# Optimization experiments

Hardware: AMD Instinct MI355X
Metric: run time of the kernel (lower is better)

The kernel has to match this reference:

```python
import jax, jax.numpy as jnp
import numpy as np

N_NODES = 50000
N_EDGES = 400000
D = 300          # num_features == hidden_units
L = 5            # num_layers
C = 128          # num_outputs
NG = 256         # graphs per batch
BN_EPS = 1e-5


def setup_inputs() -> dict:
    key = jax.random.key(0)
    ks = jax.random.split(key, 16)
    x = jax.random.normal(ks[0], (N_NODES, D), dtype=jnp.float32)
    edge_index = jax.random.randint(ks[1], (2, N_EDGES), 0, N_NODES, dtype=jnp.int64)
    batch = jnp.sort(jax.random.randint(ks[2], (N_NODES,), 0, NG, dtype=jnp.int64))
    s = 1.0 / np.sqrt(D)
    # Stacked per-layer GINConv MLP params: Linear -> BN -> ReLU -> Linear, then outer BN
    mlp_W1 = jax.random.uniform(ks[3], (L, D, D), jnp.float32, -s, s)
    mlp_b1 = jax.random.uniform(ks[4], (L, D), jnp.float32, -s, s)
    mlp_g1 = jnp.ones((L, D), jnp.float32)
    mlp_be1 = jnp.zeros((L, D), jnp.float32)
    mlp_W2 = jax.random.uniform(ks[5], (L, D, D), jnp.float32, -s, s)
    mlp_b2 = jax.random.uniform(ks[6], (L, D), jnp.float32, -s, s)
    bn_g = jnp.ones((L, D), jnp.float32)
    bn_b = jnp.zeros((L, D), jnp.float32)
    # num_layers+1 readout heads (num_features == hidden_units so all [D, C])
    fc_W = jax.random.uniform(ks[7], (L + 1, D, C), jnp.float32, -s, s)
    fc_b = jax.random.uniform(ks[8], (L + 1, C), jnp.float32, -s, s)
    return dict(x=x, edge_index=edge_index, batch=batch,
                mlp_W1=mlp_W1, mlp_b1=mlp_b1, mlp_g1=mlp_g1, mlp_be1=mlp_be1,
                mlp_W2=mlp_W2, mlp_b2=mlp_b2, bn_g=bn_g, bn_b=bn_b,
                fc_W=fc_W, fc_b=fc_b)


def _bn(h, gamma, beta):
    # BatchNorm1d in training mode: biased batch stats over the node dim
    mu = h.mean(axis=0)
    var = h.var(axis=0)
    return (h - mu) * jax.lax.rsqrt(var + BN_EPS) * gamma + beta


def reference(x, edge_index, batch, mlp_W1, mlp_b1, mlp_g1, mlp_be1,
              mlp_W2, mlp_b2, bn_g, bn_b, fc_W, fc_b):
    src, dst = edge_index[0], edge_index[1]
    n = x.shape[0]
    outs = [x]
    h = x
    for i in range(L):
        # GINConv (eps=0): MLP(x + sum_{j in N(i)} x_j), scatter-add over edges
        agg = jax.ops.segment_sum(h[src], dst, num_segments=n)
        z = h + agg
        z = z @ mlp_W1[i] + mlp_b1[i]
        z = jax.nn.relu(_bn(z, mlp_g1[i], mlp_be1[i]))
        z = z @ mlp_W2[i] + mlp_b2[i]
        h = jax.nn.relu(_bn(z, bn_g[i], bn_b[i]))  # outer BN + ReLU
        outs.append(h)
    # global mean pool per graph, then per-depth linear heads summed (dropout off in eval)
    counts = jax.ops.segment_sum(jnp.ones((n,), x.dtype), batch, num_segments=NG)
    inv = 1.0 / jnp.maximum(counts, 1.0)
    out = jnp.zeros((NG, C), x.dtype)
    for i, hi in enumerate(outs):
        pooled = jax.ops.segment_sum(hi, batch, num_segments=NG) * inv[:, None]
        out = out + (pooled @ fc_W[i] + fc_b[i])
    return out
```

## Files before the change

kernel.cpp:

```cpp
#include <hip/hip_runtime.h>

#define D 300
#define KP 320
#define NPAD 50048
#define NTILES 782
#define TPB 4
#define GB 196
#define WSTRIDE 328
#define NGR 256
#define NL 5
#define NC 128
#define BN_EPS 1e-5f

typedef __attribute__((ext_vector_type(8))) short bf16x8;
typedef __attribute__((ext_vector_type(4))) float f32x4;
typedef unsigned short u16;

__device__ __forceinline__ void atomAdd(float* p, float v) { unsafeAtomicAdd(p, v); }

__device__ __forceinline__ short f2bf(float f) {
    union { float f; unsigned u; } v; v.f = f;
    unsigned r = v.u + 0x7fffu + ((v.u >> 16) & 1u);
    return (short)(r >> 16);
}
__device__ __forceinline__ float bf2f(short s) {
    union { unsigned u; float f; } v;
    v.u = ((unsigned)(u16)s) << 16;
    return v.f;
}

__global__ void offsets_kernel(const int* __restrict__ batch, int* __restrict__ off, int N) {
    int g = threadIdx.x;
    if (g > NGR) return;
    int lo = 0, hi = N;
    while (lo < hi) {
        int mid = (lo + hi) >> 1;
        if (batch[mid] < g) lo = mid + 1; else hi = mid;
    }
    off[g] = lo;
}

__global__ __launch_bounds__(256)
void deg_kernel(const int* __restrict__ ei, int* __restrict__ deg, int E) {
    int e = blockIdx.x * 256 + threadIdx.x;
    if (e < E) atomicAdd(&deg[ei[E + e]], 1);
}

__global__ __launch_bounds__(256)
void degpart_kernel(const int* __restrict__ deg, int* __restrict__ part, int N) {
    int i = blockIdx.x * 256 + threadIdx.x;
    int v = (i < N) ? deg[i] : 0;
    #pragma unroll
    for (int o = 1; o < 64; o <<= 1) v += __shfl_xor(v, o);
    __shared__ int ws[4];
    if ((threadIdx.x & 63) == 0) ws[threadIdx.x >> 6] = v;
    __syncthreads();
    if (threadIdx.x == 0) part[blockIdx.x] = ws[0] + ws[1] + ws[2] + ws[3];
}

__global__ __launch_bounds__(256)
void partscan_kernel(int* __restrict__ part, int nb) {
    __shared__ int buf[256];
    int t = threadIdx.x;
    int v = (t < nb) ? part[t] : 0;
    buf[t] = v;
    __syncthreads();
    for (int o = 1; o < 256; o <<= 1) {
        int u = (t >= o) ? buf[t - o] : 0;
        __syncthreads();
        buf[t] += u;
        __syncthreads();
    }
    if (t < nb) part[t] = (t == 0) ? 0 : buf[t - 1];
}

__global__ __launch_bounds__(256)
void rowptr_kernel(const int* __restrict__ deg, const int* __restrict__ part,
                   int* __restrict__ rowptr, int N, int E) {
    __shared__ int buf[256];
    int b = blockIdx.x, t = threadIdx.x;
    int i = b * 256 + t;
    int v = (i < N) ? deg[i] : 0;
    buf[t] = v;
    __syncthreads();
    for (int o = 1; o < 256; o <<= 1) {
        int u = (t >= o) ? buf[t - o] : 0;
        __syncthreads();
        buf[t] += u;
        __syncthreads();
    }
    if (i < N) rowptr[i] = part[b] + buf[t] - v;
    if (b == 0 && t == 0) rowptr[N] = E;
}

__global__ __launch_bounds__(256)
void fill_kernel(const int* __restrict__ ei, const int* __restrict__ rowptr,
                 int* __restrict__ cursor, int* __restrict__ col, int E) {
    int e = blockIdx.x * 256 + threadIdx.x;
    if (e >= E) return;
    int src = ei[e];
    int dst = ei[E + e];
    int pos = atomicAdd(&cursor[dst], 1);
    col[rowptr[dst] + pos] = src;
}

__global__ __launch_bounds__(256)
void wcvt_kernel(const float* __restrict__ W1, const float* __restrict__ W2,
                 u16* __restrict__ Wt) {
    int idx = blockIdx.x * 256 + threadIdx.x;
    if (idx >= 10 * KP * 80) return;
    int n4 = idx % 80;
    int k = (idx / 80) % KP;
    int mat = idx / (80 * KP);
    const float* Wsrc = (mat < NL) ? (W1 + (size_t)mat * D * D) : (W2 + (size_t)(mat - NL) * D * D);
    float4 w = make_float4(0.f, 0.f, 0.f, 0.f);
    if (k < D && n4 < 75) w = *(const float4*)(Wsrc + (size_t)k * D + n4 * 4);
    size_t base = ((size_t)mat * 320 + n4 * 4) * KP + k;
    Wt[base]          = (u16)f2bf(w.x);
    Wt[base + KP]     = (u16)f2bf(w.y);
    Wt[base + 2 * KP] = (u16)f2bf(w.z);
    Wt[base + 3 * KP] = (u16)f2bf(w.w);
}

__global__ __launch_bounds__(256)
void xcvt_kernel(const float* __restrict__ x, u16* __restrict__ xbf, int N) {
    int idx = blockIdx.x * 256 + threadIdx.x;
    if (idx >= NPAD * 40) return;
    int row = idx / 40;
    int c8 = (idx - row * 40) * 8;
    short o[8];
    #pragma unroll
    for (int i = 0; i < 8; ++i) {
        int c = c8 + i;
        float f = (row < N && c < D) ? x[(size_t)row * D + c] : 0.f;
        o[i] = f2bf(f);
    }
    *(bf16x8*)(xbf + (size_t)row * KP + c8) = *(bf16x8*)o;
}

template<bool APPLY>
__global__ __launch_bounds__(256)
void gather_kernel(const u16* __restrict__ H, u16* __restrict__ Z,
                   const int* __restrict__ rowptr, const int* __restrict__ col,
                   const float* __restrict__ scsh, int N) {
    int idx = blockIdx.x * 256 + threadIdx.x;
    if (idx >= N * 40) return;
    int node = idx / 40;
    int c8 = (idx - node * 40) * 8;
    float sc[8], sh[8];
    if (APPLY) {
        #pragma unroll
        for (int i = 0; i < 8; ++i) { sc[i] = scsh[c8 + i]; sh[i] = scsh[KP + c8 + i]; }
    }
    int s = rowptr[node], e = rowptr[node + 1];
    bf16x8 v = *(const bf16x8*)(H + (size_t)node * KP + c8);
    float acc[8];
    #pragma unroll
    for (int i = 0; i < 8; ++i) {
        float f = bf2f(v[i]);
        acc[i] = APPLY ? fmaxf(fmaf(f, sc[i], sh[i]), 0.f) : f;
    }
    int j = s;
    for (; j + 2 <= e; j += 2) {
        int s0 = col[j], s1 = col[j + 1];
        bf16x8 w0 = *(const bf16x8*)(H + (size_t)s0 * KP + c8);
        bf16x8 w1 = *(const bf16x8*)(H + (size_t)s1 * KP + c8);
        #pragma unroll
        for (int i = 0; i < 8; ++i) {
            float f0 = bf2f(w0[i]);
            float f1 = bf2f(w1[i]);
            acc[i] += APPLY ? fmaxf(fmaf(f0, sc[i], sh[i]), 0.f) : f0;
            acc[i] += APPLY ? fmaxf(fmaf(f1, sc[i], sh[i]), 0.f) : f1;
        }
    }
    if (j < e) {
        int s0 = col[j];
        bf16x8 w0 = *(const bf16x8*)(H + (size_t)s0 * KP + c8);
        #pragma unroll
        for (int i = 0; i < 8; ++i) {
            float f0 = bf2f(w0[i]);
            acc[i] += APPLY ? fmaxf(fmaf(f0, sc[i], sh[i]), 0.f) : f0;
        }
    }
    short o[8];
    #pragma unroll
    for (int i = 0; i < 8; ++i) o[i] = f2bf(acc[i]);
    *(bf16x8*)(Z + (size_t)node * KP + c8) = *(bf16x8*)o;
}

template<bool APPLY>
__global__ __launch_bounds__(320)
void pool_kernel(const u16* __restrict__ H, const int* __restrict__ off,
                 const float* __restrict__ scsh, float* __restrict__ pooled_l) {
    __shared__ float red[8][KP];
    int t = threadIdx.x;
    int g = blockIdx.x;
    int rq = t / 40;
    int c8 = (t - rq * 40) * 8;
    float sc[8], sh[8];
    if (APPLY) {
        #pragma unroll
        for (int i = 0; i < 8; ++i) { sc[i] = scsh[c8 + i]; sh[i] = scsh[KP + c8 + i]; }
    }
    int r0 = off[g], r1 = off[g + 1];
    float a[8] = {};
    for (int r = r0 + rq; r < r1; r += 8) {
        bf16x8 v = *(const bf16x8*)(H + (size_t)r * KP + c8);
        #pragma unroll
        for (int i = 0; i < 8; ++i) {
            float f = bf2f(v[i]);
            a[i] += APPLY ? fmaxf(fmaf(f, sc[i], sh[i]), 0.f) : f;
        }
    }
    #pragma unroll
    for (int i = 0; i < 8; ++i) red[rq][c8 + i] = a[i];
    __syncthreads();
    int c = t;
    if (c < D) {
        float s = 0.f;
        #pragma unroll
        for (int j = 0; j < 8; ++j) s += red[j][c];
        pooled_l[g * D + c] = s;
    }
}

template<bool APPLY>
__global__ __launch_bounds__(256)
void mfma_gemm_kernel(const u16* __restrict__ Abf, const u16* __restrict__ Wt,
                      const float* __restrict__ bias, const float* __restrict__ scsh,
                      u16* __restrict__ Cbf, float* __restrict__ stats, int Nreal) {
    __shared__ u16 Ws[80 * WSTRIDE];
    __shared__ float lsum[80], lsq[80];
    const int tid = threadIdx.x;
    const int nBase = blockIdx.y * 80;

    {
        const u16* src = Wt + (size_t)nBase * KP;
        for (int unit = tid; unit < 80 * 40; unit += 256) {
            int n = unit / 40, kg = unit - n * 40;
            *(bf16x8*)&Ws[n * WSTRIDE + kg * 8] =
                *(const bf16x8*)(src + (size_t)n * KP + kg * 8);
        }
    }
    if (tid < 80) { lsum[tid] = 0.f; lsq[tid] = 0.f; }
    __syncthreads();

    const int wave = tid >> 6, lane = tid & 63;
    const int quad = lane >> 4, l16 = lane & 15;

    for (int t = 0; t < TPB; ++t) {
        const int tile = blockIdx.x * TPB + t;
        if (tile >= NTILES) break;
        const int mBase = tile * 64 + wave * 16;
        const u16* arow = Abf + (size_t)(mBase + l16) * KP + quad * 8;

        bf16x8 a[10];
        #pragma unroll
        for (int kc = 0; kc < 10; ++kc) a[kc] = *(const bf16x8*)(arow + kc * 32);
        if (APPLY) {
            #pragma unroll
            for (int kc = 0; kc < 10; ++kc) {
                const float* sp = scsh + kc * 32 + quad * 8;
                float4 s0 = *(const float4*)sp;
                float4 s1 = *(const float4*)(sp + 4);
                float4 h0 = *(const float4*)(sp + KP);
                float4 h1 = *(const float4*)(sp + KP + 4);
                float sc[8] = {s0.x, s0.y, s0.z, s0.w, s1.x, s1.y, s1.z, s1.w};
                float sh[8] = {h0.x, h0.y, h0.z, h0.w, h1.x, h1.y, h1.z, h1.w};
                short o[8];
                #pragma unroll
                for (int i = 0; i < 8; ++i)
                    o[i] = f2bf(fmaxf(fmaf(bf2f(a[kc][i]), sc[i], sh[i]), 0.f));
                a[kc] = *(bf16x8*)o;
            }
        }

        f32x4 acc[5] = {};
        #pragma unroll
        for (int kc = 0; kc < 10; ++kc) {
            #pragma unroll
            for (int nt = 0; nt < 5; ++nt) {
                bf16x8 b = *(const bf16x8*)&Ws[(nt * 16 + l16) * WSTRIDE + kc * 32 + quad * 8];
                acc[nt] = __builtin_amdgcn_mfma_f32_16x16x32_bf16(a[kc], b, acc[nt], 0, 0, 0);
            }
        }

        const int rbase = mBase + quad * 4;
        #pragma unroll
        for (int nt = 0; nt < 5; ++nt) {
            int nl = nt * 16 + l16;
            int colg = nBase + nl;
            if (colg >= D) continue;
            float bia = bias[colg];
            float s = 0.f, q = 0.f;
            #pragma unroll
            for (int r = 0; r < 4; ++r) {
                int row = rbase + r;
                float v = acc[nt][r] + bia;
                bool ok = row < Nreal;
                if (ok) { s += v; q = fmaf(v, v, q); }
                Cbf[(size_t)row * KP + colg] = ok ? (u16)f2bf(v) : (u16)0;
            }
            s += __shfl_xor(s, 16); s += __shfl_xor(s, 32);
            q += __shfl_xor(q, 16); q += __shfl_xor(q, 32);
            if (quad == 0) { atomicAdd(&lsum[nl], s); atomicAdd(&lsq[nl], q); }
        }
    }
    __syncthreads();
    if (tid < 80) {
        int colg = nBase + tid;
        if (colg < D) {
            atomAdd(&stats[colg], lsum[tid]);
            atomAdd(&stats[KP + colg], lsq[tid]);
        }
    }
}

__global__ void bnfin_kernel(float* __restrict__ sums, const float* __restrict__ g,
                             const float* __restrict__ be, float* __restrict__ scsh, float invN) {
    int c = threadIdx.x;
    if (c >= D) return;
    float mu = sums[c] * invN;
    float var = sums[KP + c] * invN - mu * mu;
    float s = g[c] / sqrtf(var + BN_EPS);
    scsh[c] = s;
    scsh[KP + c] = fmaf(-mu, s, be[c]);
    sums[c] = 0.f;
    sums[KP + c] = 0.f;
}

__global__ __launch_bounds__(128)
void bias_init_kernel(const float* __restrict__ fcb, float* __restrict__ out) {
    int i = blockIdx.x * 128 + threadIdx.x;
    if (i >= NGR * NC) return;
    int c = i & (NC - 1);
    float s = 0.f;
    for (int l = 0; l <= NL; ++l) s += fcb[l * NC + c];
    out[i] = s;
}

__global__ __launch_bounds__(128)
void readout_kernel(const float* __restrict__ pooled, const int* __restrict__ off,
                    const float* __restrict__ fcW, float* __restrict__ out) {
    __shared__ float sp[4][D];
    int c = threadIdx.x;
    int l = blockIdx.y;
    int g0 = blockIdx.x * 4;
    for (int i = c; i < 4 * D; i += 128) {
        int gg = i / D, k = i - gg * D;
        sp[gg][k] = pooled[((size_t)l * NGR + g0 + gg) * D + k];
    }
    __syncthreads();
    float acc[4] = {0.f, 0.f, 0.f, 0.f};
    for (int k = 0; k < D; ++k) {
        float w = fcW[((size_t)l * D + k) * NC + c];
        #pragma unroll
        for (int gg = 0; gg < 4; ++gg) acc[gg] = fmaf(sp[gg][k], w, acc[gg]);
    }
    #pragma unroll
    for (int gg = 0; gg < 4; ++gg) {
        int g = g0 + gg;
        float inv = 1.0f / fmaxf((float)(off[g + 1] - off[g]), 1.0f);
        atomAdd(&out[g * NC + c], acc[gg] * inv);
    }
}

extern "C" void kernel_launch(void* const* d_in, const int* in_sizes, int n_in,
                              void* d_out, int out_size, void* d_ws, size_t ws_size,
                              hipStream_t stream) {
    const float* x       = (const float*)d_in[0];
    const int*   ei      = (const int*)d_in[1];
    const int*   batch   = (const int*)d_in[2];
    const float* W1  = (const float*)d_in[3];
    const float* b1  = (const float*)d_in[4];
    const float* g1  = (const float*)d_in[5];
    const float* be1 = (const float*)d_in[6];
    const float* W2  = (const float*)d_in[7];
    const float* b2  = (const float*)d_in[8];
    const float* bng = (const float*)d_in[9];
    const float* bnb = (const float*)d_in[10];
    const float* fcW = (const float*)d_in[11];
    const float* fcb = (const float*)d_in[12];
    float* out = (float*)d_out;

    const int N = in_sizes[0] / D;
    const int E = in_sizes[1] / 2;
    const int nb = (N + 255) / 256;

    u16* xbf  = (u16*)d_ws;
    u16* bufA = xbf + (size_t)NPAD * KP;
    u16* bufB = bufA + (size_t)NPAD * KP;
    u16* Wt   = bufB + (size_t)NPAD * KP;
    float* pooled = (float*)(Wt + (size_t)10 * 320 * KP);
    float* stats  = pooled + (size_t)(NL + 1) * NGR * D;
    float* sc1    = stats + 2 * KP;
    float* sc2    = sc1 + 2 * KP;
    int*   off    = (int*)(sc2 + 2 * KP);
    int*   rowptr = off + NGR + 1;
    int*   cursor = rowptr + N + 1;
    int*   col    = cursor + N;
    int*   part   = col + E;

    hipMemsetAsync(stats, 0, 6 * KP * sizeof(float), stream);
    offsets_kernel<<<1, 320, 0, stream>>>(batch, off, N);
    bias_init_kernel<<<(NGR * NC + 127) / 128, 128, 0, stream>>>(fcb, out);

    hipMemsetAsync(cursor, 0, N * sizeof(int), stream);
    deg_kernel<<<(E + 255) / 256, 256, 0, stream>>>(ei, cursor, E);
    degpart_kernel<<<nb, 256, 0, stream>>>(cursor, part, N);
    partscan_kernel<<<1, 256, 0, stream>>>(part, nb);
    rowptr_kernel<<<nb, 256, 0, stream>>>(cursor, part, rowptr, N, E);
    hipMemsetAsync(cursor, 0, N * sizeof(int), stream);
    fill_kernel<<<(E + 255) / 256, 256, 0, stream>>>(ei, rowptr, cursor, col, E);

    wcvt_kernel<<<(10 * KP * 80 + 255) / 256, 256, 0, stream>>>(W1, W2, Wt);
    xcvt_kernel<<<(NPAD * 40 + 255) / 256, 256, 0, stream>>>(x, xbf, N);

    const dim3 gemm_grid(GB, 4);
    const int nd40 = N * 40;
    float invN = 1.0f / (float)N;
    const size_t WtM = (size_t)320 * KP;

    pool_kernel<false><<<NGR, 320, 0, stream>>>(xbf, off, sc2, pooled);

    u16* g = bufA;
    u16* t = bufB;
    const u16* src = xbf;
    for (int l = 0; l < NL; ++l) {
        if (l == 0)
            gather_kernel<false><<<(nd40 + 255) / 256, 256, 0, stream>>>(src, g, rowptr, col, sc2, N);
        else
            gather_kernel<true><<<(nd40 + 255) / 256, 256, 0, stream>>>(src, g, rowptr, col, sc2, N);
        mfma_gemm_kernel<false><<<gemm_grid, 256, 0, stream>>>(
            g, Wt + (size_t)l * WtM, b1 + l * D, sc1, t, stats, N);
        bnfin_kernel<<<1, 320, 0, stream>>>(stats, g1 + l * D, be1 + l * D, sc1, invN);
        mfma_gemm_kernel<true><<<gemm_grid, 256, 0, stream>>>(
            t, Wt + (size_t)(NL + l) * WtM, b2 + l * D, sc1, g, stats, N);
        bnfin_kernel<<<1, 320, 0, stream>>>(stats, bng + l * D, bnb + l * D, sc2, invN);
        pool_kernel<true><<<NGR, 320, 0, stream>>>(g, off, sc2, pooled + (size_t)(l + 1) * NGR * D);
        src = g;
        u16* tmp = g; g = t; t = tmp;
    }
    readout_kernel<<<dim3(NGR / 4, NL + 1), 128, 0, stream>>>(pooled, off, fcW, out);
}
```

Baseline: 1.094 ms.

## Process 128-row tiles per wave pair with prefetched A fragments in MFMA GEMM

The GEMM kernel now computes two 64-row groups per wave, so each B fragment loaded from LDS feeds two MFMAs. The A fragments for the next tile are loaded during the current tile's MFMA loop, and the first tile's A loads are issued before the weight staging into LDS. Scalar bf16 rounding is replaced with the v_cvt_pk_bf16_f32 packed instruction, and the launch bound requests 3 blocks per SM. The cost is higher register pressure from the doubled A and accumulator arrays, which may reduce occupancy.

```diff
diff --git a/kernel.cpp b/kernel.cpp
--- a/kernel.cpp
+++ b/kernel.cpp
@@ -3,8 +3,8 @@
 #define D 300
 #define KP 320
 #define NPAD 50048
-#define NTILES 782
-#define TPB 4
+#define NT128 391
+#define TPB 2
 #define GB 196
 #define WSTRIDE 328
 #define NGR 256
@@ -27,6 +27,11 @@
     union { unsigned u; float f; } v;
     v.u = ((unsigned)(u16)s) << 16;
     return v.f;
+}
+__device__ __forceinline__ unsigned cvtpk(float lo, float hi) {
+    unsigned r;
+    asm("v_cvt_pk_bf16_f32 %0, %1, %2" : "=v"(r) : "v"(lo), "v"(hi));
+    return r;
 }
 
 __global__ void offsets_kernel(const int* __restrict__ batch, int* __restrict__ off, int N) {
@@ -225,7 +230,7 @@
 }
 
 template<bool APPLY>
-__global__ __launch_bounds__(256)
+__global__ __launch_bounds__(256, 3)
 void mfma_gemm_kernel(const u16* __restrict__ Abf, const u16* __restrict__ Wt,
                       const float* __restrict__ bias, const float* __restrict__ scsh,
                       u16* __restrict__ Cbf, float* __restrict__ stats, int Nreal) {
@@ -233,6 +238,17 @@
     __shared__ float lsum[80], lsq[80];
     const int tid = threadIdx.x;
     const int nBase = blockIdx.y * 80;
+    const int wave = tid >> 6, lane = tid & 63;
+    const int quad = lane >> 4, l16 = lane & 15;
+
+    const int tile0 = blockIdx.x * TPB;
+    const u16* pA = Abf + (size_t)(tile0 * 128 + wave * 16 + l16) * KP + quad * 8;
+    bf16x8 a[2][10];
+    #pragma unroll
+    for (int kc = 0; kc < 10; ++kc) {
+        a[0][kc] = *(const bf16x8*)(pA + kc * 32);
+        a[1][kc] = *(const bf16x8*)(pA + (size_t)64 * KP + kc * 32);
+    }
 
     {
         const u16* src = Wt + (size_t)nBase * KP;
@@ -245,18 +261,12 @@
     if (tid < 80) { lsum[tid] = 0.f; lsq[tid] = 0.f; }
     __syncthreads();
 
-    const int wave = tid >> 6, lane = tid & 63;
-    const int quad = lane >> 4, l16 = lane & 15;
-
+    const size_t adv = (tile0 + 1 < NT128) ? (size_t)128 * KP : 0;
+
+    #pragma unroll
     for (int t = 0; t < TPB; ++t) {
-        const int tile = blockIdx.x * TPB + t;
-        if (tile >= NTILES) break;
-        const int mBase = tile * 64 + wave * 16;
-        const u16* arow = Abf + (size_t)(mBase + l16) * KP + quad * 8;
-
-        bf16x8 a[10];
-        #pragma unroll
-        for (int kc = 0; kc < 10; ++kc) a[kc] = *(const bf16x8*)(arow + kc * 32);
+        const int tile = tile0 + t;
+
         if (APPLY) {
             #pragma unroll
             for (int kc = 0; kc < 10; ++kc) {
@@ -267,43 +277,68 @@
                 float4 h1 = *(const float4*)(sp + KP + 4);
                 float sc[8] = {s0.x, s0.y, s0.z, s0.w, s1.x, s1.y, s1.z, s1.w};
                 float sh[8] = {h0.x, h0.y, h0.z, h0.w, h1.x, h1.y, h1.z, h1.w};
-                short o[8];
                 #pragma unroll
-                for (int i = 0; i < 8; ++i)
-                    o[i] = f2bf(fmaxf(fmaf(bf2f(a[kc][i]), sc[i], sh[i]), 0.f));
-                a[kc] = *(bf16x8*)o;
+                for (int g = 0; g < 2; ++g) {
+                    float f[8];
+                    #pragma unroll
+                    for (int i = 0; i < 8; ++i)
+                        f[i] = fmaxf(fmaf(bf2f(a[g][kc][i]), sc[i], sh[i]), 0.f);
+                    union { unsigned u[4]; bf16x8 v; } o;
+                    o.u[0] = cvtpk(f[0], f[1]);
+                    o.u[1] = cvtpk(f[2], f[3]);
+                    o.u[2] = cvtpk(f[4], f[5]);
+                    o.u[3] = cvtpk(f[6], f[7]);
+                    a[g][kc] = o.v;
+                }
             }
         }
 
-        f32x4 acc[5] = {};
+        f32x4 acc[2][5] = {};
         #pragma unroll
         for (int kc = 0; kc < 10; ++kc) {
             #pragma unroll
             for (int nt = 0; nt < 5; ++nt) {
                 bf16x8 b = *(const bf16x8*)&Ws[(nt * 16 + l16) * WSTRIDE + kc * 32 + quad * 8];
-                acc[nt] = __builtin_amdgcn_mfma_f32_16x16x32_bf16(a[kc], b, acc[nt], 0, 0, 0);
+                acc[0][nt] = __builtin_amdgcn_mfma_f32_16x16x32_bf16(a[0][kc], b, acc[0][nt], 0, 0, 0);
+                acc[1][nt] = __builtin_amdgcn_mfma_f32_16x16x32_bf16(a[1][kc], b, acc[1][nt], 0, 0, 0);
             }
-        }
-
-        const int rbase = mBase + quad * 4;
-        #pragma unroll
-        for (int nt = 0; nt < 5; ++nt) {
-            int nl = nt * 16 + l16;
-            int colg = nBase + nl;
-            if (colg >= D) continue;
-            float bia = bias[colg];
-            float s = 0.f, q = 0.f;
+            if (t == 0) {
+                a[0][kc] = *(const bf16x8*)(pA + adv + kc * 32);
+                a[1][kc] = *(const bf16x8*)(pA + adv + (size_t)64 * KP + kc * 32);
+            }
+        }
+
+        if (tile < NT128) {
+            const int rb = tile * 128 + wave * 16 + quad * 4;
             #pragma unroll
-            for (int r = 0; r < 4; ++r) {
-                int row = rbase + r;
-                float v = acc[nt][r] + bia;
-                bool ok = row < Nreal;
-                if (ok) { s += v; q = fmaf(v, v, q); }
-                Cbf[(size_t)row * KP + colg] = ok ? (u16)f2bf(v) : (u16)0;
+            for (int nt = 0; nt < 5; ++nt) {
+                const int nl = nt * 16 + l16;
+                const int colg = nBase + nl;
+                if (colg < D) {
+                    const float bia = bias[colg];
+                    float s = 0.f, q = 0.f;
+                    #pragma unroll
+                    for (int g = 0; g < 2; ++g) {
+                        const int rg = rb + g * 64;
+                        #pragma unroll
+                        for (int rp = 0; rp < 2; ++rp) {
+                            const int row0 = rg + rp * 2;
+                            float v0 = acc[g][nt][rp * 2]     + bia;
+                            float v1 = acc[g][nt][rp * 2 + 1] + bia;
+                            if (row0 >= Nreal)     v0 = 0.f;
+                            if (row0 + 1 >= Nreal) v1 = 0.f;
+                            s += v0 + v1;
+                            q = fmaf(v0, v0, fmaf(v1, v1, q));
+                            const unsigned pk = cvtpk(v0, v1);
+                            Cbf[(size_t)row0 * KP + colg]       = (u16)(pk & 0xffffu);
+                            Cbf[(size_t)(row0 + 1) * KP + colg] = (u16)(pk >> 16);
+                        }
+                    }
+                    s += __shfl_xor(s, 16); s += __shfl_xor(s, 32);
+                    q += __shfl_xor(q, 16); q += __shfl_xor(q, 32);
+                    if (quad == 0) { atomicAdd(&lsum[nl], s); atomicAdd(&lsq[nl], q); }
+                }
             }
-            s += __shfl_xor(s, 16); s += __shfl_xor(s, 32);
-            q += __shfl_xor(q, 16); q += __shfl_xor(q, 32);
-            if (quad == 0) { atomicAdd(&lsum[nl], s); atomicAdd(&lsq[nl], q); }
         }
     }
     __syncthreads();
```

Result: faster. 1.038 ms (-5.1%).

## Restructure MFMA GEMM: weights in registers, double-buffered A tiles via LDS DMA

Applied to the files above, without the earlier changes.

The GEMM kernel now keeps each wave's 16-column weight slice in registers and streams 64-row activation tiles into swizzled, double-buffered LDS with global_load_lds, prefetching the next tile while computing the current one. It uses 5 waves (320 threads) so the 80 output columns split across waves, applies the BN+ReLU transform once per staged tile in LDS, and packs results with v_cvt_pk_bf16_f32. BN statistics are accumulated in registers and reduced with DPP row shifts before the global atomics, replacing the LDS atomics. The aim is to cut repeated weight reads from LDS and hide global load latency, at the cost of higher register pressure and an extra barrier per tile on the APPLY path.

```diff
diff --git a/kernel.cpp b/kernel.cpp
--- a/kernel.cpp
+++ b/kernel.cpp
@@ -3,10 +3,9 @@
 #define D 300
 #define KP 320
 #define NPAD 50048
-#define NTILES 782
-#define TPB 4
-#define GB 196
-#define WSTRIDE 328
+#define NT64 782
+#define TPBT 4
+#define GBX 196
 #define NGR 256
 #define NL 5
 #define NC 128
@@ -27,6 +26,27 @@
     union { unsigned u; float f; } v;
     v.u = ((unsigned)(u16)s) << 16;
     return v.f;
+}
+__device__ __forceinline__ unsigned cvtpk(float lo, float hi) {
+    unsigned r;
+    asm("v_cvt_pk_bf16_f32 %0, %1, %2" : "=v"(r) : "v"(lo), "v"(hi));
+    return r;
+}
+template<int C>
+__device__ __forceinline__ float rs_add(float v) {
+    int x = __builtin_amdgcn_update_dpp(0, __float_as_int(v), C, 0xF, 0xF, true);
+    return v + __int_as_float(x);
+}
+__device__ __forceinline__ float red16(float v) {
+    v = rs_add<0x111>(v);
+    v = rs_add<0x112>(v);
+    v = rs_add<0x114>(v);
+    v = rs_add<0x118>(v);
+    return v;
+}
+__device__ __forceinline__ void gload_lds16(const u16* g, u16* l) {
+    __builtin_amdgcn_global_load_lds((const __attribute__((address_space(1))) void*)g,
+                                     (__attribute__((address_space(3))) void*)l, 16, 0, 0);
 }
 
 __global__ void offsets_kernel(const int* __restrict__ batch, int* __restrict__ off, int N) {
@@ -225,93 +245,121 @@
 }
 
 template<bool APPLY>
-__global__ __launch_bounds__(256)
+__global__ __launch_bounds__(320, 3)
 void mfma_gemm_kernel(const u16* __restrict__ Abf, const u16* __restrict__ Wt,
                       const float* __restrict__ bias, const float* __restrict__ scsh,
                       u16* __restrict__ Cbf, float* __restrict__ stats, int Nreal) {
-    __shared__ u16 Ws[80 * WSTRIDE];
-    __shared__ float lsum[80], lsq[80];
-    const int tid = threadIdx.x;
-    const int nBase = blockIdx.y * 80;
-
-    {
-        const u16* src = Wt + (size_t)nBase * KP;
-        for (int unit = tid; unit < 80 * 40; unit += 256) {
-            int n = unit / 40, kg = unit - n * 40;
-            *(bf16x8*)&Ws[n * WSTRIDE + kg * 8] =
-                *(const bf16x8*)(src + (size_t)n * KP + kg * 8);
-        }
-    }
-    if (tid < 80) { lsum[tid] = 0.f; lsq[tid] = 0.f; }
-    __syncthreads();
-
+    __shared__ u16 Ab[2][64 * 320];
+    const int tid  = threadIdx.x;
     const int wave = tid >> 6, lane = tid & 63;
     const int quad = lane >> 4, l16 = lane & 15;
-
-    for (int t = 0; t < TPB; ++t) {
-        const int tile = blockIdx.x * TPB + t;
-        if (tile >= NTILES) break;
-        const int mBase = tile * 64 + wave * 16;
-        const u16* arow = Abf + (size_t)(mBase + l16) * KP + quad * 8;
-
-        bf16x8 a[10];
-        #pragma unroll
-        for (int kc = 0; kc < 10; ++kc) a[kc] = *(const bf16x8*)(arow + kc * 32);
+    const int nW   = blockIdx.y * 80 + wave * 16;
+    const int tile0 = blockIdx.x * TPBT;
+
+    bf16x8 bw[10];
+    {
+        const u16* wp = Wt + (size_t)(nW + l16) * KP + quad * 8;
+        #pragma unroll
+        for (int kc = 0; kc < 10; ++kc) bw[kc] = *(const bf16x8*)(wp + kc * 32);
+    }
+    const int c0 = nW + quad * 4;
+    float bia[4];
+    #pragma unroll
+    for (int r = 0; r < 4; ++r) bia[r] = (c0 + r < D) ? bias[c0 + r] : 0.f;
+
+    float rsc[8], rsh[8];
+    if (APPLY) {
+        const int k0 = (((tid % 40) ^ ((tid / 40) & 7))) * 8;
+        #pragma unroll
+        for (int i = 0; i < 8; ++i) { rsc[i] = scsh[k0 + i]; rsh[i] = scsh[KP + k0 + i]; }
+    }
+
+    auto stage = [&](int buf, int tile) {
+        const size_t rowb = (size_t)tile * 64;
+        #pragma unroll
+        for (int i = 0; i < 8; ++i) {
+            int chunk = i * 320 + tid;
+            int r  = chunk / 40;
+            int cc = chunk - r * 40;
+            int off = (cc * 16) ^ ((r & 7) << 4);
+            gload_lds16(Abf + (rowb + r) * KP + (off >> 1), &Ab[buf][chunk * 8]);
+        }
+    };
+
+    stage(0, tile0);
+    __syncthreads();
+
+    float sl[4] = {0.f, 0.f, 0.f, 0.f}, ql[4] = {0.f, 0.f, 0.f, 0.f};
+    int cur = 0;
+
+    for (int i = 0; i < TPBT; ++i) {
+        const int tile = tile0 + i;
+        if (tile >= NT64) break;
+        if (i + 1 < TPBT && tile + 1 < NT64) stage(cur ^ 1, tile + 1);
+
         if (APPLY) {
             #pragma unroll
-            for (int kc = 0; kc < 10; ++kc) {
-                const float* sp = scsh + kc * 32 + quad * 8;
-                float4 s0 = *(const float4*)sp;
-                float4 s1 = *(const float4*)(sp + 4);
-                float4 h0 = *(const float4*)(sp + KP);
-                float4 h1 = *(const float4*)(sp + KP + 4);
-                float sc[8] = {s0.x, s0.y, s0.z, s0.w, s1.x, s1.y, s1.z, s1.w};
-                float sh[8] = {h0.x, h0.y, h0.z, h0.w, h1.x, h1.y, h1.z, h1.w};
-                short o[8];
+            for (int u = 0; u < 8; ++u) {
+                const int chunk = u * 320 + tid;
+                bf16x8 v = *(const bf16x8*)&Ab[cur][chunk * 8];
+                float f[8];
                 #pragma unroll
-                for (int i = 0; i < 8; ++i)
-                    o[i] = f2bf(fmaxf(fmaf(bf2f(a[kc][i]), sc[i], sh[i]), 0.f));
-                a[kc] = *(bf16x8*)o;
+                for (int j = 0; j < 8; ++j)
+                    f[j] = fmaxf(fmaf(bf2f(v[j]), rsc[j], rsh[j]), 0.f);
+                union { unsigned w[4]; bf16x8 v; } o;
+                o.w[0] = cvtpk(f[0], f[1]);
+                o.w[1] = cvtpk(f[2], f[3]);
+                o.w[2] = cvtpk(f[4], f[5]);
+                o.w[3] = cvtpk(f[6], f[7]);
+                *(bf16x8*)&Ab[cur][chunk * 8] = o.v;
             }
-        }
-
-        f32x4 acc[5] = {};
+            asm volatile("s_waitcnt lgkmcnt(0)" ::: "memory");
+            __builtin_amdgcn_sched_barrier(0);
+            __builtin_amdgcn_s_barrier();
+        }
+
+        f32x4 acc[4] = {};
         #pragma unroll
         for (int kc = 0; kc < 10; ++kc) {
             #pragma unroll
-            for (int nt = 0; nt < 5; ++nt) {
-                bf16x8 b = *(const bf16x8*)&Ws[(nt * 16 + l16) * WSTRIDE + kc * 32 + quad * 8];
-                acc[nt] = __builtin_amdgcn_mfma_f32_16x16x32_bf16(a[kc], b, acc[nt], 0, 0, 0);
+            for (int rg = 0; rg < 4; ++rg) {
+                const int row = rg * 16 + l16;
+                const int off = (kc * 64 + quad * 16) ^ ((l16 & 7) << 4);
+                bf16x8 af = *(const bf16x8*)&Ab[cur][row * 320 + (off >> 1)];
+                acc[rg] = __builtin_amdgcn_mfma_f32_16x16x32_bf16(bw[kc], af, acc[rg], 0, 0, 0);
             }
         }
 
-        const int rbase = mBase + quad * 4;
-        #pragma unroll
-        for (int nt = 0; nt < 5; ++nt) {
-            int nl = nt * 16 + l16;
-            int colg = nBase + nl;
-            if (colg >= D) continue;
-            float bia = bias[colg];
-            float s = 0.f, q = 0.f;
+        const int rowb = tile * 64;
+        u16* cr = Cbf + (size_t)(rowb + l16) * KP + c0;
+        #pragma unroll
+        for (int rg = 0; rg < 4; ++rg) {
+            float v[4];
+            #pragma unroll
+            for (int r = 0; r < 4; ++r) v[r] = acc[rg][r] + bia[r];
+            uint2 w;
+            w.x = cvtpk(v[0], v[1]);
+            w.y = cvtpk(v[2], v[3]);
+            *(uint2*)(cr + (size_t)(rg * 16) * KP) = w;
+            const bool ok = (rowb + rg * 16 + l16) < Nreal;
             #pragma unroll
             for (int r = 0; r < 4; ++r) {
-                int row = rbase + r;
-                float v = acc[nt][r] + bia;
-                bool ok = row < Nreal;
-                if (ok) { s += v; q = fmaf(v, v, q); }
-                Cbf[(size_t)row * KP + colg] = ok ? (u16)f2bf(v) : (u16)0;
+                float s0 = ok ? v[r] : 0.f;
+                sl[r] += s0;
+                ql[r] = fmaf(s0, s0, ql[r]);
             }
-            s += __shfl_xor(s, 16); s += __shfl_xor(s, 32);
-            q += __shfl_xor(q, 16); q += __shfl_xor(q, 32);
-            if (quad == 0) { atomicAdd(&lsum[nl], s); atomicAdd(&lsq[nl], q); }
-        }
-    }
-    __syncthreads();
-    if (tid < 80) {
-        int colg = nBase + tid;
-        if (colg < D) {
-            atomAdd(&stats[colg], lsum[tid]);
-            atomAdd(&stats[KP + colg], lsq[tid]);
+        }
+        __syncthreads();
+        cur ^= 1;
+    }
+
+    #pragma unroll
+    for (int r = 0; r < 4; ++r) {
+        float sv = red16(sl[r]);
+        float qv = red16(ql[r]);
+        if (l16 == 15 && c0 + r < D) {
+            atomAdd(&stats[c0 + r], sv);
+            atomAdd(&stats[KP + c0 + r], qv);
         }
     }
 }
@@ -416,7 +464,7 @@
     wcvt_kernel<<<(10 * KP * 80 + 255) / 256, 256, 0, stream>>>(W1, W2, Wt);
     xcvt_kernel<<<(NPAD * 40 + 255) / 256, 256, 0, stream>>>(x, xbf, N);
 
-    const dim3 gemm_grid(GB, 4);
+    const dim3 gemm_grid(GBX, 4);
     const int nd40 = N * 40;
     float invN = 1.0f / (float)N;
     const size_t WtM = (size_t)320 * KP;
@@ -431,10 +479,10 @@
             gather_kernel<false><<<(nd40 + 255) / 256, 256, 0, stream>>>(src, g, rowptr, col, sc2, N);
         else
             gather_kernel<true><<<(nd40 + 255) / 256, 256, 0, stream>>>(src, g, rowptr, col, sc2, N);
-        mfma_gemm_kernel<false><<<gemm_grid, 256, 0, stream>>>(
+        mfma_gemm_kernel<false><<<gemm_grid, 320, 0, stream>>>(
             g, Wt + (size_t)l * WtM, b1 + l * D, sc1, t, stats, N);
         bnfin_kernel<<<1, 320, 0, stream>>>(stats, g1 + l * D, be1 + l * D, sc1, invN);
-        mfma_gemm_kernel<true><<<gemm_grid, 256, 0, stream>>>(
+        mfma_gemm_kernel<true><<<gemm_grid, 320, 0, stream>>>(
             t, Wt + (size_t)(NL + l) * WtM, b2 + l * D, sc1, g, stats, N);
         bnfin_kernel<<<1, 320, 0, stream>>>(stats, bng + l * D, bnb + l * D, sc2, invN);
         pool_kernel<true><<<NGR, 320, 0, stream>>>(g, off, sc2, pooled + (size_t)(l + 1) * NGR * D);
```

Result: slower. 1.304 ms (+19.2%).
